# Optimization experiments

Measured on AMD Instinct MI355X. Metric: run time of the kernel, lower is better.

Reference implementation:

```python
import jax, jax.numpy as jnp
import numpy as np

D_MODEL = 1024
NUM_HEADS = 16
D_K = D_MODEL // NUM_HEADS
B, S = 4, 2048


def setup_inputs() -> dict:
    key = jax.random.key(0)
    ks = jax.random.split(key, 7)
    scale = 1.0 / np.sqrt(D_MODEL)
    query = jax.random.normal(ks[0], (B, S, D_MODEL), dtype=jnp.float32)
    k_in = jax.random.normal(ks[1], (B, S, D_MODEL), dtype=jnp.float32)
    value = jax.random.normal(ks[2], (B, S, D_MODEL), dtype=jnp.float32)
    # causal mask: 1 where attention allowed, 0 where blocked
    mask = jnp.tril(jnp.ones((S, S), dtype=jnp.int32))[None, None, :, :]
    w_q = jax.random.normal(ks[3], (D_MODEL, D_MODEL), dtype=jnp.float32) * scale
    w_k = jax.random.normal(ks[4], (D_MODEL, D_MODEL), dtype=jnp.float32) * scale
    w_v = jax.random.normal(ks[5], (D_MODEL, D_MODEL), dtype=jnp.float32) * scale
    w_o = jax.random.normal(ks[6], (D_MODEL, D_MODEL), dtype=jnp.float32) * scale
    return {"query": query, "key": k_in, "value": value, "mask": mask,
            "w_q": w_q, "w_k": w_k, "w_v": w_v, "w_o": w_o}


def reference(query, key, value, mask, w_q, w_k, w_v, w_o):
    # nn.Linear(d, d, bias=False): y = x @ W.T
    q = query @ w_q.T
    k = key @ w_k.T
    v = value @ w_v.T
    # [B, S, D] -> [B, H, S, d_k]
    def split_heads(x):
        return x.reshape(B, S, NUM_HEADS, D_K).transpose(0, 2, 1, 3)
    q, k, v = split_heads(q), split_heads(k), split_heads(v)
    scores = jnp.einsum('bhqd,bhkd->bhqk', q, k) / jnp.sqrt(jnp.float32(D_K))
    scores = jnp.where(mask == 0, jnp.float32(-1e9), scores)
    attn = jax.nn.softmax(scores, axis=-1)  # dropout p=0.0 -> identity
    x = jnp.einsum('bhqk,bhkd->bhqd', attn, v)
    x = x.transpose(0, 2, 1, 3).reshape(B, S, D_MODEL)
    return x @ w_o.T
```

## Files before the change

### kernel.cpp

```cpp
#include <hip/hip_runtime.h>
#include <stdint.h>

#define S_LEN 2048
#define NH 16
#define DKH 64
#define NB 4
#define DM 1024
#define MROWS (NB * S_LEN)

typedef __attribute__((ext_vector_type(4))) float f32x4;
typedef __attribute__((ext_vector_type(8))) short bf16x8;
typedef __attribute__((ext_vector_type(4))) unsigned int u32x4;

static __device__ __forceinline__ unsigned short f2bf(float x) {
    unsigned int u = __builtin_bit_cast(unsigned int, x);
    return (unsigned short)((u + 0x7FFFu + ((u >> 16) & 1u)) >> 16);
}
static __device__ __forceinline__ unsigned int pack2bf(float lo, float hi) {
    return (unsigned int)f2bf(lo) | ((unsigned int)f2bf(hi) << 16);
}

static __device__ __forceinline__ void gld_lds16(const void* g, void* lds) {
    auto gp = (const __attribute__((address_space(1))) unsigned int*)(uintptr_t)(g);
    auto lp = (__attribute__((address_space(3))) unsigned int*)(uintptr_t)(lds);
    __builtin_amdgcn_global_load_lds(gp, lp, 16, 0, 0);
}

__global__ __launch_bounds__(256) void cvt3_f32_bf16(
    const float* __restrict__ i0, const float* __restrict__ i1, const float* __restrict__ i2,
    unsigned short* __restrict__ o0, unsigned short* __restrict__ o1, unsigned short* __restrict__ o2,
    int nvec)
{
    const float* in = (blockIdx.z == 0) ? i0 : (blockIdx.z == 1) ? i1 : i2;
    unsigned short* out = (blockIdx.z == 0) ? o0 : (blockIdx.z == 1) ? o1 : o2;
    const int stride = gridDim.x * blockDim.x;
    for (int i = blockIdx.x * blockDim.x + threadIdx.x; i < nvec; i += stride) {
        float4 v = ((const float4*)in)[i];
        ushort4 r;
        r.x = f2bf(v.x); r.y = f2bf(v.y); r.z = f2bf(v.z); r.w = f2bf(v.w);
        ((ushort4*)out)[i] = r;
    }
}

__global__ __launch_bounds__(256) void cvt4_f32_bf16(
    const float* __restrict__ i0, const float* __restrict__ i1, const float* __restrict__ i2, const float* __restrict__ i3,
    unsigned short* __restrict__ o0, unsigned short* __restrict__ o1, unsigned short* __restrict__ o2, unsigned short* __restrict__ o3,
    int nvec)
{
    const float* in = (blockIdx.z == 0) ? i0 : (blockIdx.z == 1) ? i1 : (blockIdx.z == 2) ? i2 : i3;
    unsigned short* out = (blockIdx.z == 0) ? o0 : (blockIdx.z == 1) ? o1 : (blockIdx.z == 2) ? o2 : o3;
    const int stride = gridDim.x * blockDim.x;
    for (int i = blockIdx.x * blockDim.x + threadIdx.x; i < nvec; i += stride) {
        float4 v = ((const float4*)in)[i];
        ushort4 r;
        r.x = f2bf(v.x); r.y = f2bf(v.y); r.z = f2bf(v.z); r.w = f2bf(v.w);
        ((ushort4*)out)[i] = r;
    }
}

template <int MODE>
__global__ __launch_bounds__(256) void gemm_bt(
    const unsigned short* __restrict__ A0, const unsigned short* __restrict__ A1, const unsigned short* __restrict__ A2,
    const unsigned short* __restrict__ B0, const unsigned short* __restrict__ B1, const unsigned short* __restrict__ B2,
    void* __restrict__ C0, void* __restrict__ C1, void* __restrict__ C2, float qscale)
{
    __shared__ __align__(16) unsigned short As[128 * 64];
    __shared__ __align__(16) unsigned short Bs[128 * 64];

    const int nwg = gridDim.x * gridDim.y * gridDim.z;
    const int bid = blockIdx.x + gridDim.x * (blockIdx.y + gridDim.y * blockIdx.z);
    const int swz = (bid & 7) * (nwg >> 3) + (bid >> 3);
    const int bx = swz & 7;
    const int by = (swz >> 3) & 63;
    const int bz = swz >> 9;

    const unsigned short* A = (bz == 0) ? A0 : (bz == 1) ? A1 : A2;
    const unsigned short* B = (bz == 0) ? B0 : (bz == 1) ? B1 : B2;
    void* C = (bz == 0) ? C0 : (bz == 1) ? C1 : C2;
    const float cscale = (MODE == 1 && bz == 0) ? qscale : 1.0f;

    const int t = threadIdx.x;
    const int w = t >> 6, l = t & 63;
    const int wr = w >> 1, wc = w & 1;
    const int m0 = by * 128, n0 = bx * 128;

    f32x4 acc[4][4] = {};

    const int srow = t >> 3, schp = t & 7;
    const int scol = ((schp ^ (srow & 7)) << 3);
    const unsigned short* Ag = A + (size_t)(m0 + srow) * 1024 + scol;
    const unsigned short* Bg = B + (size_t)(n0 + srow) * 1024 + scol;
    unsigned short* AsW = &As[w * 512];
    unsigned short* BsW = &Bs[w * 512];

    for (int kt = 0; kt < 16; ++kt) {
        __syncthreads();
        const int kb = kt * 64;
#pragma unroll
        for (int i = 0; i < 4; ++i) {
            gld_lds16(Ag + (size_t)i * 32 * 1024 + kb, AsW + i * 2048);
            gld_lds16(Bg + (size_t)i * 32 * 1024 + kb, BsW + i * 2048);
        }
        __syncthreads();
#pragma unroll
        for (int kk = 0; kk < 2; ++kk) {
            const int koff = (((kk * 4 + (l >> 4)) ^ (l & 7)) << 3);
            bf16x8 af[4], bfr[4];
#pragma unroll
            for (int m = 0; m < 4; ++m)
                af[m] = *(const bf16x8*)&As[(wr * 64 + m * 16 + (l & 15)) * 64 + koff];
#pragma unroll
            for (int n = 0; n < 4; ++n)
                bfr[n] = *(const bf16x8*)&Bs[(wc * 64 + n * 16 + (l & 15)) * 64 + koff];
#pragma unroll
            for (int m = 0; m < 4; ++m)
#pragma unroll
                for (int n = 0; n < 4; ++n)
                    acc[m][n] = __builtin_amdgcn_mfma_f32_16x16x32_bf16(af[m], bfr[n], acc[m][n], 0, 0, 0);
        }
    }

#pragma unroll
    for (int m = 0; m < 4; ++m) {
#pragma unroll
        for (int n = 0; n < 4; ++n) {
            const int rowb = m0 + wr * 64 + m * 16 + (l >> 4) * 4;
            const int col  = n0 + wc * 64 + n * 16 + (l & 15);
            if (MODE == 1 && bz == 2) {
                const int bh = (rowb >> 11) * 16 + (col >> 6);
                const int dk = col & 63;
                const int s0 = rowb & 2047;
                const unsigned int w0 = pack2bf(acc[m][n][0], acc[m][n][1]);
                const unsigned int w1 = pack2bf(acc[m][n][2], acc[m][n][3]);
                *(uint2*)&((unsigned short*)C)[((size_t)bh * 64 + dk) * 2048 + s0] = make_uint2(w0, w1);
            } else {
#pragma unroll
                for (int r = 0; r < 4; ++r) {
                    const int row = rowb + r;
                    if (MODE == 1) {
                        ((unsigned short*)C)[(size_t)((row >> 11) * 16 + (col >> 6)) * (S_LEN * 64) +
                                             (size_t)(row & 2047) * 64 + (col & 63)] = f2bf(acc[m][n][r] * cscale);
                    } else {
                        ((float*)C)[(size_t)row * 1024 + col] = acc[m][n][r];
                    }
                }
            }
        }
    }
}

__global__ __launch_bounds__(512, 4) void attn_fwd(
    const unsigned short* __restrict__ Qh, const unsigned short* __restrict__ Kh,
    const unsigned short* __restrict__ Vth, unsigned short* __restrict__ Ao)
{
    __shared__ __align__(16) unsigned short Kts[2 * 4096];
    __shared__ __align__(16) unsigned short Vts[2 * 4096];

    const int t = threadIdx.x, w = t >> 6, l = t & 63;
    const int g = l >> 4, c = l & 15;
    const int bid = blockIdx.x;
    const int qi = 15 - (bid >> 6);
    const int bh = bid & 63;
    const int b = bh >> 4, h = bh & 15;
    const int q0 = qi * 128;

    const unsigned short* Qg  = Qh  + (size_t)bh * (S_LEN * 64);
    const unsigned short* Kg  = Kh  + (size_t)bh * (S_LEN * 64);
    const unsigned short* Vtg = Vth + (size_t)bh * (64 * S_LEN);

    const int qrow = q0 + w * 16 + c;
    const unsigned short* Qp = Qg + (size_t)qrow * 64 + g * 8;
    bf16x8 qf[2];
    qf[0] = *(const bf16x8*)(Qp);
    qf[1] = *(const bf16x8*)(Qp + 32);

    const int krow = t >> 3, kchp = t & 7;
    const unsigned short* Ksrc = Kg + (size_t)krow * 64 + ((kchp ^ (krow & 7)) << 3);
    const unsigned short* Vsrc = Vtg + (size_t)(t >> 3) * 2048 + ((kchp ^ ((t >> 3) & 7)) << 3);
    const int ldsW = w * 512;

    float m_run = -1e30f, l_run = 0.0f;
    f32x4 oacc[4] = {};

    const int ntile = 2 * qi + 2;
    gld_lds16(Ksrc, &Kts[ldsW]);
    gld_lds16(Vsrc, &Vts[ldsW]);

    for (int kv = 0; kv < ntile; ++kv) {
        const int kv0 = kv * 64;
        __syncthreads();

        if (kv + 1 < ntile) {
            const int nb4 = ((kv + 1) & 1) * 4096;
            gld_lds16(Ksrc + (size_t)(kv0 + 64) * 64, &Kts[nb4 + ldsW]);
            gld_lds16(Vsrc + (kv0 + 64), &Vts[nb4 + ldsW]);
        }

        if (kv0 > q0 + w * 16 + 15) continue;

        const unsigned short* Kb = &Kts[(kv & 1) * 4096];
        const unsigned short* Vb = &Vts[(kv & 1) * 4096];

        f32x4 sc[4] = {};
#pragma unroll
        for (int kk = 0; kk < 2; ++kk) {
#pragma unroll
            for (int nb = 0; nb < 4; ++nb) {
                const int row = nb * 16 + c;
                const int chp = (kk * 4 + g) ^ (c & 7);
                const bf16x8 kfr = *(const bf16x8*)&Kb[row * 64 + chp * 8];
                sc[nb] = __builtin_amdgcn_mfma_f32_16x16x32_bf16(kfr, qf[kk], sc[nb], 0, 0, 0);
            }
        }

        if (kv >= ntile - 2) {
#pragma unroll
            for (int nb = 0; nb < 4; ++nb)
#pragma unroll
                for (int r = 0; r < 4; ++r)
                    if (kv0 + nb * 16 + 4 * g + r > qrow) sc[nb][r] = -1e30f;
        }

        float mx = -1e30f;
#pragma unroll
        for (int nb = 0; nb < 4; ++nb)
#pragma unroll
            for (int r = 0; r < 4; ++r) mx = fmaxf(mx, sc[nb][r]);
        mx = fmaxf(mx, __shfl_xor(mx, 16));
        mx = fmaxf(mx, __shfl_xor(mx, 32));

        if (!__all(mx - m_run <= 8.0f)) {
            const float mnew = fmaxf(m_run, mx);
            const float alpha = __expf(m_run - mnew);
            m_run = mnew;
            float af[4];
#pragma unroll
            for (int r = 0; r < 4; ++r) af[r] = __shfl(alpha, 4 * g + r);
#pragma unroll
            for (int db = 0; db < 4; ++db)
#pragma unroll
                for (int r = 0; r < 4; ++r) oacc[db][r] *= af[r];
            l_run *= alpha;
        }

        float s = 0.0f;
#pragma unroll
        for (int nb = 0; nb < 4; ++nb)
#pragma unroll
            for (int r = 0; r < 4; ++r) {
                const float p = __expf(sc[nb][r] - m_run);
                sc[nb][r] = p;
                s += p;
            }
        s += __shfl_xor(s, 16);
        s += __shfl_xor(s, 32);
        l_run += s;

        unsigned int pk[4][2];
#pragma unroll
        for (int nb = 0; nb < 4; ++nb) {
            pk[nb][0] = pack2bf(sc[nb][0], sc[nb][1]);
            pk[nb][1] = pack2bf(sc[nb][2], sc[nb][3]);
        }
        const int srcA = 32 * (g & 1) + c;
        const int srcB = srcA + 16;
        const bool hi = (g >= 2);
        unsigned int apw[2][4];
#pragma unroll
        for (int kk2 = 0; kk2 < 2; ++kk2) {
            const unsigned int a0 = __shfl(pk[2 * kk2][0], srcA), b0 = __shfl(pk[2 * kk2 + 1][0], srcA);
            const unsigned int a1 = __shfl(pk[2 * kk2][1], srcA), b1 = __shfl(pk[2 * kk2 + 1][1], srcA);
            const unsigned int a2 = __shfl(pk[2 * kk2][0], srcB), b2 = __shfl(pk[2 * kk2 + 1][0], srcB);
            const unsigned int a3 = __shfl(pk[2 * kk2][1], srcB), b3 = __shfl(pk[2 * kk2 + 1][1], srcB);
            apw[kk2][0] = hi ? b0 : a0;
            apw[kk2][1] = hi ? b1 : a1;
            apw[kk2][2] = hi ? b2 : a2;
            apw[kk2][3] = hi ? b3 : a3;
        }

#pragma unroll
        for (int kk2 = 0; kk2 < 2; ++kk2) {
            const bf16x8 ap = __builtin_bit_cast(bf16x8, *(const u32x4*)apw[kk2]);
#pragma unroll
            for (int db = 0; db < 4; ++db) {
                const int d = db * 16 + c;
                const int chp = (kk2 * 4 + g) ^ (d & 7);
                const bf16x8 bv = *(const bf16x8*)&Vb[d * 64 + chp * 8];
                oacc[db] = __builtin_amdgcn_mfma_f32_16x16x32_bf16(ap, bv, oacc[db], 0, 0, 0);
            }
        }
    }

    float li[4];
#pragma unroll
    for (int r = 0; r < 4; ++r) li[r] = __shfl(l_run, 4 * g + r);
#pragma unroll
    for (int db = 0; db < 4; ++db)
#pragma unroll
        for (int r = 0; r < 4; ++r) {
            const int sq = q0 + w * 16 + 4 * g + r;
            const int col = h * 64 + db * 16 + c;
            Ao[(size_t)b * (S_LEN * 1024) + (size_t)sq * 1024 + col] = f2bf(oacc[db][r] / li[r]);
        }
}

extern "C" void kernel_launch(void* const* d_in, const int* in_sizes, int n_in,
                              void* d_out, int out_size, void* d_ws, size_t ws_size,
                              hipStream_t stream) {
    (void)in_sizes; (void)n_in; (void)out_size; (void)ws_size;
    const float* q_in = (const float*)d_in[0];
    const float* k_in = (const float*)d_in[1];
    const float* v_in = (const float*)d_in[2];
    const float* w_q = (const float*)d_in[4];
    const float* w_k = (const float*)d_in[5];
    const float* w_v = (const float*)d_in[6];
    const float* w_o = (const float*)d_in[7];

    const size_t NELEM = (size_t)MROWS * 1024;
    unsigned short* qb  = (unsigned short*)d_ws;
    unsigned short* kb  = qb + NELEM;
    unsigned short* vb  = kb + NELEM;
    unsigned short* wqb = vb + NELEM;
    unsigned short* wkb = wqb + 1024 * 1024;
    unsigned short* wvb = wkb + 1024 * 1024;
    unsigned short* wob = wvb + 1024 * 1024;
    unsigned short* Qhp = wob + 1024 * 1024;
    unsigned short* Khp = Qhp + NELEM;
    unsigned short* Vtp = Khp + NELEM;
    unsigned short* Aop = qb;

    cvt3_f32_bf16<<<dim3(1024, 1, 3), 256, 0, stream>>>(q_in, k_in, v_in, qb, kb, vb, (int)(NELEM / 4));
    cvt4_f32_bf16<<<dim3(256, 1, 4), 256, 0, stream>>>(w_q, w_k, w_v, w_o, wqb, wkb, wvb, wob, 1024 * 1024 / 4);

    gemm_bt<1><<<dim3(8, 64, 3), 256, 0, stream>>>(qb, kb, vb, wqb, wkb, wvb, Qhp, Khp, Vtp, 0.125f);
    attn_fwd<<<dim3(1024), 512, 0, stream>>>(Qhp, Khp, Vtp, Aop);
    gemm_bt<2><<<dim3(8, 64, 1), 256, 0, stream>>>(Aop, nullptr, nullptr, wob, nullptr, nullptr,
                                                   d_out, nullptr, nullptr, 1.0f);
}
```

Before: 326.1 us.

## Fuse fp32-to-bf16 activation conversion into QKV projection GEMM A-tile loads

Removes the separate activation conversion kernel. The QKV GEMM now loads fp32 activations through registers, converts them with the hardware packed bf16 convert instruction, and stores them into swizzled LDS. This saves writing and re-reading three bf16 activation copies. It also replaces the software round-to-nearest bf16 packing with v_cvt_pk_bf16_f32 in the epilogue and the attention kernel. The trade-off is that the A tile now takes a register path instead of direct global-to-LDS loads, and each A load moves twice as many bytes.

After: 330.6 us. About the same (+1.4%).

```diff
diff --git a/kernel.cpp b/kernel.cpp
--- a/kernel.cpp
+++ b/kernel.cpp
@@ -16,30 +16,16 @@
     unsigned int u = __builtin_bit_cast(unsigned int, x);
     return (unsigned short)((u + 0x7FFFu + ((u >> 16) & 1u)) >> 16);
 }
-static __device__ __forceinline__ unsigned int pack2bf(float lo, float hi) {
-    return (unsigned int)f2bf(lo) | ((unsigned int)f2bf(hi) << 16);
+static __device__ __forceinline__ unsigned int cvtpk(float lo, float hi) {
+    unsigned int r;
+    asm("v_cvt_pk_bf16_f32 %0, %1, %2" : "=v"(r) : "v"(lo), "v"(hi));
+    return r;
 }
 
 static __device__ __forceinline__ void gld_lds16(const void* g, void* lds) {
     auto gp = (const __attribute__((address_space(1))) unsigned int*)(uintptr_t)(g);
     auto lp = (__attribute__((address_space(3))) unsigned int*)(uintptr_t)(lds);
     __builtin_amdgcn_global_load_lds(gp, lp, 16, 0, 0);
-}
-
-__global__ __launch_bounds__(256) void cvt3_f32_bf16(
-    const float* __restrict__ i0, const float* __restrict__ i1, const float* __restrict__ i2,
-    unsigned short* __restrict__ o0, unsigned short* __restrict__ o1, unsigned short* __restrict__ o2,
-    int nvec)
-{
-    const float* in = (blockIdx.z == 0) ? i0 : (blockIdx.z == 1) ? i1 : i2;
-    unsigned short* out = (blockIdx.z == 0) ? o0 : (blockIdx.z == 1) ? o1 : o2;
-    const int stride = gridDim.x * blockDim.x;
-    for (int i = blockIdx.x * blockDim.x + threadIdx.x; i < nvec; i += stride) {
-        float4 v = ((const float4*)in)[i];
-        ushort4 r;
-        r.x = f2bf(v.x); r.y = f2bf(v.y); r.z = f2bf(v.z); r.w = f2bf(v.w);
-        ((ushort4*)out)[i] = r;
-    }
 }
 
 __global__ __launch_bounds__(256) void cvt4_f32_bf16(
@@ -60,7 +46,7 @@
 
 template <int MODE>
 __global__ __launch_bounds__(256) void gemm_bt(
-    const unsigned short* __restrict__ A0, const unsigned short* __restrict__ A1, const unsigned short* __restrict__ A2,
+    const void* __restrict__ A0, const void* __restrict__ A1, const void* __restrict__ A2,
     const unsigned short* __restrict__ B0, const unsigned short* __restrict__ B1, const unsigned short* __restrict__ B2,
     void* __restrict__ C0, void* __restrict__ C1, void* __restrict__ C2, float qscale)
 {
@@ -74,7 +60,7 @@
     const int by = (swz >> 3) & 63;
     const int bz = swz >> 9;
 
-    const unsigned short* A = (bz == 0) ? A0 : (bz == 1) ? A1 : A2;
+    const void* Av = (bz == 0) ? A0 : (bz == 1) ? A1 : A2;
     const unsigned short* B = (bz == 0) ? B0 : (bz == 1) ? B1 : B2;
     void* C = (bz == 0) ? C0 : (bz == 1) ? C1 : C2;
     const float cscale = (MODE == 1 && bz == 0) ? qscale : 1.0f;
@@ -88,18 +74,42 @@
 
     const int srow = t >> 3, schp = t & 7;
     const int scol = ((schp ^ (srow & 7)) << 3);
-    const unsigned short* Ag = A + (size_t)(m0 + srow) * 1024 + scol;
     const unsigned short* Bg = B + (size_t)(n0 + srow) * 1024 + scol;
+    unsigned short* BsW = &Bs[w * 512];
+    const unsigned short* Ag16 = (const unsigned short*)Av + (size_t)(m0 + srow) * 1024 + scol;
     unsigned short* AsW = &As[w * 512];
-    unsigned short* BsW = &Bs[w * 512];
+    const float* Ag32 = (const float*)Av + (size_t)(m0 + srow) * 1024 + schp * 8;
+    unsigned short* AsD = &As[srow * 64 + ((schp ^ (srow & 7)) << 3)];
 
     for (int kt = 0; kt < 16; ++kt) {
         __syncthreads();
         const int kb = kt * 64;
-#pragma unroll
-        for (int i = 0; i < 4; ++i) {
-            gld_lds16(Ag + (size_t)i * 32 * 1024 + kb, AsW + i * 2048);
-            gld_lds16(Bg + (size_t)i * 32 * 1024 + kb, BsW + i * 2048);
+        if constexpr (MODE == 1) {
+            float4 v0[4], v1[4];
+#pragma unroll
+            for (int i = 0; i < 4; ++i) {
+                const float* p = Ag32 + (size_t)i * 32 * 1024 + kb;
+                v0[i] = *(const float4*)p;
+                v1[i] = *(const float4*)(p + 4);
+            }
+#pragma unroll
+            for (int i = 0; i < 4; ++i)
+                gld_lds16(Bg + (size_t)i * 32 * 1024 + kb, BsW + i * 2048);
+#pragma unroll
+            for (int i = 0; i < 4; ++i) {
+                u32x4 pk4;
+                pk4[0] = cvtpk(v0[i].x, v0[i].y);
+                pk4[1] = cvtpk(v0[i].z, v0[i].w);
+                pk4[2] = cvtpk(v1[i].x, v1[i].y);
+                pk4[3] = cvtpk(v1[i].z, v1[i].w);
+                *(u32x4*)(AsD + i * 2048) = pk4;
+            }
+        } else {
+#pragma unroll
+            for (int i = 0; i < 4; ++i) {
+                gld_lds16(Ag16 + (size_t)i * 32 * 1024 + kb, AsW + i * 2048);
+                gld_lds16(Bg + (size_t)i * 32 * 1024 + kb, BsW + i * 2048);
+            }
         }
         __syncthreads();
 #pragma unroll
@@ -130,8 +140,8 @@
                 const int bh = (rowb >> 11) * 16 + (col >> 6);
                 const int dk = col & 63;
                 const int s0 = rowb & 2047;
-                const unsigned int w0 = pack2bf(acc[m][n][0], acc[m][n][1]);
-                const unsigned int w1 = pack2bf(acc[m][n][2], acc[m][n][3]);
+                const unsigned int w0 = cvtpk(acc[m][n][0], acc[m][n][1]);
+                const unsigned int w1 = cvtpk(acc[m][n][2], acc[m][n][3]);
                 *(uint2*)&((unsigned short*)C)[((size_t)bh * 64 + dk) * 2048 + s0] = make_uint2(w0, w1);
             } else {
 #pragma unroll
@@ -259,8 +269,8 @@
         unsigned int pk[4][2];
 #pragma unroll
         for (int nb = 0; nb < 4; ++nb) {
-            pk[nb][0] = pack2bf(sc[nb][0], sc[nb][1]);
-            pk[nb][1] = pack2bf(sc[nb][2], sc[nb][3]);
+            pk[nb][0] = cvtpk(sc[nb][0], sc[nb][1]);
+            pk[nb][1] = cvtpk(sc[nb][2], sc[nb][3]);
         }
         const int srcA = 32 * (g & 1) + c;
         const int srcB = srcA + 16;
@@ -317,22 +327,18 @@
     const float* w_o = (const float*)d_in[7];
 
     const size_t NELEM = (size_t)MROWS * 1024;
-    unsigned short* qb  = (unsigned short*)d_ws;
-    unsigned short* kb  = qb + NELEM;
-    unsigned short* vb  = kb + NELEM;
-    unsigned short* wqb = vb + NELEM;
+    unsigned short* wqb = (unsigned short*)d_ws;
     unsigned short* wkb = wqb + 1024 * 1024;
     unsigned short* wvb = wkb + 1024 * 1024;
     unsigned short* wob = wvb + 1024 * 1024;
     unsigned short* Qhp = wob + 1024 * 1024;
     unsigned short* Khp = Qhp + NELEM;
     unsigned short* Vtp = Khp + NELEM;
-    unsigned short* Aop = qb;
-
-    cvt3_f32_bf16<<<dim3(1024, 1, 3), 256, 0, stream>>>(q_in, k_in, v_in, qb, kb, vb, (int)(NELEM / 4));
+    unsigned short* Aop = Vtp + NELEM;
+
     cvt4_f32_bf16<<<dim3(256, 1, 4), 256, 0, stream>>>(w_q, w_k, w_v, w_o, wqb, wkb, wvb, wob, 1024 * 1024 / 4);
 
-    gemm_bt<1><<<dim3(8, 64, 3), 256, 0, stream>>>(qb, kb, vb, wqb, wkb, wvb, Qhp, Khp, Vtp, 0.125f);
+    gemm_bt<1><<<dim3(8, 64, 3), 256, 0, stream>>>(q_in, k_in, v_in, wqb, wkb, wvb, Qhp, Khp, Vtp, 0.125f);
     attn_fwd<<<dim3(1024), 512, 0, stream>>>(Qhp, Khp, Vtp, Aop);
     gemm_bt<2><<<dim3(8, 64, 1), 256, 0, stream>>>(Aop, nullptr, nullptr, wob, nullptr, nullptr,
                                                    d_out, nullptr, nullptr, 1.0f);
```
